# Optimization experiments

Hardware: AMD Instinct MI355X
Metric: run time of the kernel (lower is better)

Reference implementation:

```python
import jax, jax.numpy as jnp
import numpy as np

N_NODES = 98304
N_EDGES = 1572864
HIDDEN = 64
N_COMM = 128


def setup_inputs() -> dict:
    key = jax.random.key(0)
    ks = jax.random.split(key, 9)
    return {
        "x_real": jax.random.normal(ks[0], (N_NODES, 1), dtype=jnp.float32),
        "x_imag": jax.random.normal(ks[1], (N_NODES, 1), dtype=jnp.float32),
        "edge_index": jax.random.randint(ks[2], (2, N_EDGES), 0, N_NODES),
        "edge_weight": jax.random.normal(ks[3], (N_EDGES,), dtype=jnp.float32),
        "comm_id": jax.random.randint(ks[4], (N_NODES,), 0, N_COMM),
        "W_local_r": jax.random.normal(ks[5], (HIDDEN, 1), dtype=jnp.float32) * 0.5,
        "W_local_i": jax.random.normal(ks[6], (HIDDEN, 1), dtype=jnp.float32) * 0.5,
        "W_global_r": jax.random.normal(ks[7], (HIDDEN, 1), dtype=jnp.float32) * 0.5,
        "W_global_i": jax.random.normal(ks[8], (HIDDEN, 1), dtype=jnp.float32) * 0.5,
    }


def reference(x_real, x_imag, edge_index, edge_weight, comm_id,
              W_local_r, W_local_i, W_global_r, W_global_i):
    """IntraInterCommunityBlock forward (combine='sum'), complex math as (real, imag) pairs.

    CommunityGNN (1 layer, no bias): complex Linear -> weighted scatter-add
    message passing -> CSiLU (SiLU applied independently to real and imag parts).
    Residual skipped because in_channels=1 != hidden (shape mismatch in source).
    Edge split by community is implemented by zero-masking edge weights, which is
    exactly equivalent for sum aggregation (message = w * x_j).
    """
    n = x_real.shape[0]
    src, dst = edge_index[0], edge_index[1]
    same = comm_id[src] == comm_id[dst]
    ew_intra = jnp.where(same, edge_weight, 0.0)
    ew_inter = jnp.where(same, 0.0, edge_weight)

    def gnn(Wr, Wi, ew):
        # complex linear: (Wr + iWi)(xr + i xi)
        hr = x_real @ Wr.T - x_imag @ Wi.T  # [N, H]
        hi = x_real @ Wi.T + x_imag @ Wr.T  # [N, H]
        # gather -> weight -> scatter-add (aggr='add')
        mr = ew[:, None] * hr[src]  # [E, H]
        mi = ew[:, None] * hi[src]
        ar = jax.ops.segment_sum(mr, dst, num_segments=n)
        ai = jax.ops.segment_sum(mi, dst, num_segments=n)
        # CSiLU: SiLU on real and imag parts
        return jax.nn.silu(ar), jax.nn.silu(ai)

    lr, li = gnn(W_local_r, W_local_i, ew_intra)
    gr, gi = gnn(W_global_r, W_global_i, ew_inter)
    # combine='sum'; stack real/imag on last axis -> [N, H, 2]
    return jnp.stack([lr + gr, li + gi], axis=-1)
```

## Files before the change

### kernel.cpp

```cpp
#include <hip/hip_runtime.h>

#define N_NODES 98304
#define N_EDGES 1572864
#define HIDDEN  64

#define NB      1536
#define NBLK    1536
#define CHUNK   1024
#define TPB     256
#define EPT     4
#define NBXC    (NB / 8)

#define FP_SCALE 1048576.0f
#define FP_INV   (1.0f / 1048576.0f)

__device__ __forceinline__ float silu_f(float x) {
    return x / (1.0f + __expf(-x));
}

__global__ __launch_bounds__(TPB) void prep_kernel(const float* __restrict__ xr,
                                                   const float* __restrict__ xi,
                                                   const int* __restrict__ comm,
                                                   float4* __restrict__ node)
{
    const int n = blockIdx.x * TPB + threadIdx.x;
    if (n < N_NODES) {
        float4 v;
        v.x = xr[n];
        v.y = xi[n];
        v.z = __int_as_float(comm[n]);
        v.w = 0.0f;
        node[n] = v;
    }
}

__global__ __launch_bounds__(TPB) void k_scatter(const int* __restrict__ ei,
    const float* __restrict__ ew, const float4* __restrict__ node,
    const int* __restrict__ comm,
    unsigned short* __restrict__ lbT, unsigned long long* __restrict__ payload)
{
    __shared__ unsigned long long sorted[CHUNK];
    __shared__ unsigned hist[NB];
    __shared__ unsigned localbase[NB];

    const int tid = threadIdx.x, blk = blockIdx.x;
    for (int i = tid; i < NB; i += TPB) hist[i] = 0;
    __syncthreads();

    const int ebase = blk * CHUNK;
    unsigned long long pay[EPT];
    unsigned pb[EPT], pr[EPT];
#pragma unroll
    for (int k = 0; k < EPT; ++k) {
        const int e = ebase + k * TPB + tid;
        const int s = ei[e];
        const int d = ei[N_EDGES + e];
        const float w = ew[e];
        const float4 ns = node[s];
        const int cd = comm[d];
        const int dr = __float2int_rn(w * ns.x * FP_SCALE);
        const int di = __float2int_rn(w * ns.y * FP_SCALE);
        const unsigned flag = (__float_as_int(ns.z) == cd) ? 0u : 1u;
        const unsigned b = (unsigned)d >> 6;
        pb[k] = b;
        pr[k] = atomicAdd(&hist[b], 1u);
        pay[k] = ((unsigned long long)((unsigned)dr & 0x07FFFFFFu) << 37)
               | ((unsigned long long)((unsigned)di & 0x07FFFFFFu) << 10)
               | ((unsigned long long)((unsigned)(d & 63)) << 4)
               | ((unsigned long long)flag << 1);
    }
    __syncthreads();

    if (tid < 64) {
        unsigned v[24];
        unsigned s = 0;
#pragma unroll
        for (int m = 0; m < 24; ++m) { v[m] = hist[tid * 24 + m]; s += v[m]; }
        unsigned p = s;
#pragma unroll
        for (int off = 1; off < 64; off <<= 1) {
            unsigned t = __shfl_up(p, off);
            if (tid >= off) p += t;
        }
        unsigned excl = p - s;
#pragma unroll
        for (int m = 0; m < 24; ++m) { unsigned t = v[m]; localbase[tid * 24 + m] = excl; excl += t; }
    }
    __syncthreads();

#pragma unroll
    for (int k = 0; k < EPT; ++k)
        sorted[localbase[pb[k]] + pr[k]] = pay[k];
    for (int i = tid; i < NB; i += TPB)
        lbT[(size_t)blk * NB + i] = (unsigned short)localbase[i];
    __syncthreads();

    const ulonglong2* src2 = (const ulonglong2*)sorted;
    ulonglong2* dst2 = (ulonglong2*)(payload + (size_t)blk * CHUNK);
#pragma unroll
    for (int i = tid; i < CHUNK / 2; i += TPB)
        dst2[i] = src2[i];
}

__global__ __launch_bounds__(TPB) void k_accum_final(
    const unsigned long long* __restrict__ payload,
    const unsigned short* __restrict__ lbT,
    const float* __restrict__ Wlr, const float* __restrict__ Wli,
    const float* __restrict__ Wgr, const float* __restrict__ Wgi,
    float4* __restrict__ out)
{
    __shared__ int accR[128];
    __shared__ int accI[128];
    __shared__ float2 w_s[4][32];
    const int tid = threadIdx.x, blk = blockIdx.x;
    const int bucket = (blk & 7) * NBXC + (blk >> 3);

    if (tid < 128) { accR[tid] = 0; accI[tid] = 0; }
    else {
        const int t = tid - 128;
        const int which = t >> 5, h2 = t & 31;
        const float* W = (which == 0) ? Wlr : (which == 1) ? Wli
                       : (which == 2) ? Wgr : Wgi;
        w_s[which][h2] = ((const float2*)W)[h2];
    }
    __syncthreads();

    for (int c = tid; c < NBLK; c += TPB) {
        const unsigned start = lbT[(size_t)c * NB + bucket];
        const unsigned end   = (bucket < NB - 1)
                             ? (unsigned)lbT[(size_t)c * NB + bucket + 1]
                             : (unsigned)CHUNK;
        const unsigned long long* chunkp = payload + (size_t)c * CHUNK;
        for (unsigned i = start; i < end; ++i) {
            const unsigned long long p = chunkp[i];
            const int dr = (int)((long long)p >> 37);
            const int di = (int)(((long long)(p << 27)) >> 37);
            const unsigned idx = (((unsigned)(p >> 4) & 63u) << 1) | ((unsigned)(p >> 1) & 1u);
            atomicAdd(&accR[idx], dr);
            atomicAdd(&accI[idx], di);
        }
    }
    __syncthreads();

    const size_t obase = (size_t)bucket * 2048;
#pragma unroll
    for (int jj = 0; jj < 8; ++jj) {
        const int idx = jj * 256 + tid;
        const int ln  = idx >> 5;
        const int h2  = idx & 31;
        const float sr_l = (float)accR[ln * 2 + 0] * FP_INV;
        const float si_l = (float)accI[ln * 2 + 0] * FP_INV;
        const float sr_g = (float)accR[ln * 2 + 1] * FP_INV;
        const float si_g = (float)accI[ln * 2 + 1] * FP_INV;
        const float2 a = w_s[0][h2], c = w_s[1][h2];
        const float2 g = w_s[2][h2], f = w_s[3][h2];
        float4 o;
        {
            const float arl = a.x * sr_l - c.x * si_l;
            const float ail = c.x * sr_l + a.x * si_l;
            const float arg = g.x * sr_g - f.x * si_g;
            const float aig = f.x * sr_g + g.x * si_g;
            o.x = silu_f(arl) + silu_f(arg);
            o.y = silu_f(ail) + silu_f(aig);
        }
        {
            const float arl = a.y * sr_l - c.y * si_l;
            const float ail = c.y * sr_l + a.y * si_l;
            const float arg = g.y * sr_g - f.y * si_g;
            const float aig = f.y * sr_g + g.y * si_g;
            o.z = silu_f(arl) + silu_f(arg);
            o.w = silu_f(ail) + silu_f(aig);
        }
        out[obase + idx] = o;
    }
}

__global__ void edge_scatter_fb(const int* __restrict__ ei,
                                const float* __restrict__ ew,
                                const int* __restrict__ comm,
                                const float* __restrict__ xr,
                                const float* __restrict__ xi,
                                unsigned long long* __restrict__ P)
{
    const int e = blockIdx.x * blockDim.x + threadIdx.x;
    if (e >= N_EDGES) return;
    const int s = ei[e];
    const int d = ei[N_EDGES + e];
    const float w = ew[e];
    const int dr = __float2int_rn(w * xr[s] * FP_SCALE);
    const int di = __float2int_rn(w * xi[s] * FP_SCALE);
    const unsigned long long delta =
        (unsigned long long)(((long long)dr << 32) + (long long)di);
    const int base = (comm[s] == comm[d]) ? 0 : N_NODES;
    atomicAdd(&P[base + d], delta);
}

__global__ void epilogue_fb(const unsigned long long* __restrict__ P,
                            const float* __restrict__ Wlr,
                            const float* __restrict__ Wli,
                            const float* __restrict__ Wgr,
                            const float* __restrict__ Wgi,
                            float4* __restrict__ out)
{
    const int total = N_NODES * (HIDDEN / 2);
    const int t = blockIdx.x * blockDim.x + threadIdx.x;
    if (t >= total) return;
    const int n = t >> 5, h2 = t & 31;
    float sr_l, si_l, sr_g, si_g;
    {
        const unsigned long long U = P[n];
        const int bi = (int)(unsigned)(U & 0xffffffffULL);
        const int ar = (int)(unsigned)(U >> 32) + (bi < 0 ? 1 : 0);
        sr_l = (float)ar * FP_INV; si_l = (float)bi * FP_INV;
    }
    {
        const unsigned long long U = P[N_NODES + n];
        const int bi = (int)(unsigned)(U & 0xffffffffULL);
        const int ar = (int)(unsigned)(U >> 32) + (bi < 0 ? 1 : 0);
        sr_g = (float)ar * FP_INV; si_g = (float)bi * FP_INV;
    }
    const float2 wlr = ((const float2*)Wlr)[h2];
    const float2 wli = ((const float2*)Wli)[h2];
    const float2 wgr = ((const float2*)Wgr)[h2];
    const float2 wgi = ((const float2*)Wgi)[h2];
    float4 o;
    {
        const float arl = wlr.x * sr_l - wli.x * si_l;
        const float ail = wli.x * sr_l + wlr.x * si_l;
        const float arg = wgr.x * sr_g - wgi.x * si_g;
        const float aig = wgi.x * sr_g + wgr.x * si_g;
        o.x = silu_f(arl) + silu_f(arg);
        o.y = silu_f(ail) + silu_f(aig);
    }
    {
        const float arl = wlr.y * sr_l - wli.y * si_l;
        const float ail = wli.y * sr_l + wlr.y * si_l;
        const float arg = wgr.y * sr_g - wgi.y * si_g;
        const float aig = wgi.y * sr_g + wgr.y * si_g;
        o.z = silu_f(arl) + silu_f(arg);
        o.w = silu_f(ail) + silu_f(aig);
    }
    out[t] = o;
}

extern "C" void kernel_launch(void* const* d_in, const int* in_sizes, int n_in,
                              void* d_out, int out_size, void* d_ws, size_t ws_size,
                              hipStream_t stream) {
    const float* xr   = (const float*)d_in[0];
    const float* xi   = (const float*)d_in[1];
    const int*   ei   = (const int*)d_in[2];
    const float* ew   = (const float*)d_in[3];
    const int*   comm = (const int*)d_in[4];
    const float* Wlr  = (const float*)d_in[5];
    const float* Wli  = (const float*)d_in[6];
    const float* Wgr  = (const float*)d_in[7];
    const float* Wgi  = (const float*)d_in[8];

    const size_t payload_bytes = (size_t)N_EDGES * sizeof(unsigned long long);
    const size_t lbT_bytes     = (size_t)NBLK * NB * sizeof(unsigned short);
    const size_t node_bytes    = (size_t)N_NODES * sizeof(float4);
    const size_t need = payload_bytes + lbT_bytes + node_bytes;

    if (ws_size >= need) {
        char* p = (char*)d_ws;
        unsigned long long* payload = (unsigned long long*)p;  p += payload_bytes;
        unsigned short* lbT         = (unsigned short*)p;      p += lbT_bytes;
        float4* node                = (float4*)p;

        hipLaunchKernelGGL(prep_kernel, dim3(N_NODES / TPB), dim3(TPB), 0, stream,
                           xr, xi, comm, node);
        hipLaunchKernelGGL(k_scatter, dim3(NBLK), dim3(TPB), 0, stream,
                           ei, ew, node, comm, lbT, payload);
        hipLaunchKernelGGL(k_accum_final, dim3(NB), dim3(TPB), 0, stream,
                           payload, lbT, Wlr, Wli, Wgr, Wgi, (float4*)d_out);
    } else {
        unsigned long long* P = (unsigned long long*)d_ws;
        hipMemsetAsync(P, 0, (size_t)2 * N_NODES * sizeof(unsigned long long), stream);
        hipLaunchKernelGGL(edge_scatter_fb, dim3((N_EDGES + 255) / 256), dim3(256), 0, stream,
                           ei, ew, comm, xr, xi, P);
        const int total = N_NODES * (HIDDEN / 2);
        hipLaunchKernelGGL(epilogue_fb, dim3((total + 255) / 256), dim3(256), 0, stream,
                           P, Wlr, Wli, Wgr, Wgi, (float4*)d_out);
    }
}
```

Before: 64.72 us.

## Transpose bucket offsets into packed rows and drop node-packing prep kernel

Adds a transpose kernel that turns the per-chunk bucket offset table into per-bucket rows, packing start and count into one 16-bit word. The accumulate kernel then reads its bucket's row contiguously instead of doing strided loads across chunks, and skips empty chunks early. It also removes the prep kernel that packed nodes into float4, gathering xr, xi and comm directly in the scatter kernel, and uses nontemporal loads for the edge streams. In exchange there is an extra kernel launch, more uncoalesced gathers in the scatter kernel, and a fallback read of the original table when a count saturates.

```diff
diff --git a/kernel.cpp b/kernel.cpp
--- a/kernel.cpp
+++ b/kernel.cpp
@@ -18,25 +18,9 @@
     return x / (1.0f + __expf(-x));
 }
 
-__global__ __launch_bounds__(TPB) void prep_kernel(const float* __restrict__ xr,
-                                                   const float* __restrict__ xi,
-                                                   const int* __restrict__ comm,
-                                                   float4* __restrict__ node)
-{
-    const int n = blockIdx.x * TPB + threadIdx.x;
-    if (n < N_NODES) {
-        float4 v;
-        v.x = xr[n];
-        v.y = xi[n];
-        v.z = __int_as_float(comm[n]);
-        v.w = 0.0f;
-        node[n] = v;
-    }
-}
-
 __global__ __launch_bounds__(TPB) void k_scatter(const int* __restrict__ ei,
-    const float* __restrict__ ew, const float4* __restrict__ node,
-    const int* __restrict__ comm,
+    const float* __restrict__ ew, const float* __restrict__ xr,
+    const float* __restrict__ xi, const int* __restrict__ comm,
     unsigned short* __restrict__ lbT, unsigned long long* __restrict__ payload)
 {
     __shared__ unsigned long long sorted[CHUNK];
@@ -53,14 +37,12 @@
 #pragma unroll
     for (int k = 0; k < EPT; ++k) {
         const int e = ebase + k * TPB + tid;
-        const int s = ei[e];
-        const int d = ei[N_EDGES + e];
-        const float w = ew[e];
-        const float4 ns = node[s];
-        const int cd = comm[d];
-        const int dr = __float2int_rn(w * ns.x * FP_SCALE);
-        const int di = __float2int_rn(w * ns.y * FP_SCALE);
-        const unsigned flag = (__float_as_int(ns.z) == cd) ? 0u : 1u;
+        const int s = __builtin_nontemporal_load(&ei[e]);
+        const int d = __builtin_nontemporal_load(&ei[N_EDGES + e]);
+        const float w = __builtin_nontemporal_load(&ew[e]);
+        const int dr = __float2int_rn(w * xr[s] * FP_SCALE);
+        const int di = __float2int_rn(w * xi[s] * FP_SCALE);
+        const unsigned flag = (comm[s] == comm[d]) ? 0u : 1u;
         const unsigned b = (unsigned)d >> 6;
         pb[k] = b;
         pr[k] = atomicAdd(&hist[b], 1u);
@@ -102,8 +84,38 @@
         dst2[i] = src2[i];
 }
 
+__global__ __launch_bounds__(TPB) void k_transpose(
+    const unsigned short* __restrict__ lbT,
+    unsigned short* __restrict__ lbTT)
+{
+    __shared__ unsigned short t[64][66];
+    const int b0 = blockIdx.x * 64;
+    const int c0 = blockIdx.y * 64;
+    const int tid = threadIdx.x;
+
+    for (int idx = tid; idx < 64 * 65; idx += TPB) {
+        const int r  = idx / 65;
+        const int cb = idx % 65;
+        const int gb = b0 + cb;
+        t[r][cb] = (gb < NB) ? lbT[(size_t)(c0 + r) * NB + gb]
+                             : (unsigned short)CHUNK;
+    }
+    __syncthreads();
+
+    for (int idx = tid; idx < 64 * 64; idx += TPB) {
+        const int col = idx >> 6;
+        const int r   = idx & 63;
+        const unsigned start = t[r][col];
+        unsigned cnt = (unsigned)t[r][col + 1] - start;
+        if (cnt > 63u) cnt = 63u;
+        const unsigned pk = cnt ? ((start << 6) | cnt) : 0u;
+        lbTT[(size_t)(b0 + col) * NBLK + (c0 + r)] = (unsigned short)pk;
+    }
+}
+
 __global__ __launch_bounds__(TPB) void k_accum_final(
     const unsigned long long* __restrict__ payload,
+    const unsigned short* __restrict__ lbTT,
     const unsigned short* __restrict__ lbT,
     const float* __restrict__ Wlr, const float* __restrict__ Wli,
     const float* __restrict__ Wgr, const float* __restrict__ Wgi,
@@ -125,11 +137,17 @@
     }
     __syncthreads();
 
+    const unsigned short* row = lbTT + (size_t)bucket * NBLK;
     for (int c = tid; c < NBLK; c += TPB) {
-        const unsigned start = lbT[(size_t)c * NB + bucket];
-        const unsigned end   = (bucket < NB - 1)
-                             ? (unsigned)lbT[(size_t)c * NB + bucket + 1]
-                             : (unsigned)CHUNK;
+        const unsigned pk = row[c];
+        if (pk == 0u) continue;
+        const unsigned start = pk >> 6;
+        unsigned end = start + (pk & 63u);
+        if ((pk & 63u) == 63u) {
+            end = (bucket < NB - 1)
+                ? (unsigned)lbT[(size_t)c * NB + bucket + 1]
+                : (unsigned)CHUNK;
+        }
         const unsigned long long* chunkp = payload + (size_t)c * CHUNK;
         for (unsigned i = start; i < end; ++i) {
             const unsigned long long p = chunkp[i];
@@ -258,21 +276,21 @@
 
     const size_t payload_bytes = (size_t)N_EDGES * sizeof(unsigned long long);
     const size_t lbT_bytes     = (size_t)NBLK * NB * sizeof(unsigned short);
-    const size_t node_bytes    = (size_t)N_NODES * sizeof(float4);
-    const size_t need = payload_bytes + lbT_bytes + node_bytes;
+    const size_t lbTT_bytes    = (size_t)NB * NBLK * sizeof(unsigned short);
+    const size_t need = payload_bytes + lbT_bytes + lbTT_bytes;
 
     if (ws_size >= need) {
         char* p = (char*)d_ws;
         unsigned long long* payload = (unsigned long long*)p;  p += payload_bytes;
         unsigned short* lbT         = (unsigned short*)p;      p += lbT_bytes;
-        float4* node                = (float4*)p;
-
-        hipLaunchKernelGGL(prep_kernel, dim3(N_NODES / TPB), dim3(TPB), 0, stream,
-                           xr, xi, comm, node);
+        unsigned short* lbTT        = (unsigned short*)p;
+
         hipLaunchKernelGGL(k_scatter, dim3(NBLK), dim3(TPB), 0, stream,
-                           ei, ew, node, comm, lbT, payload);
+                           ei, ew, xr, xi, comm, lbT, payload);
+        hipLaunchKernelGGL(k_transpose, dim3(NB / 64, NBLK / 64), dim3(TPB), 0, stream,
+                           lbT, lbTT);
         hipLaunchKernelGGL(k_accum_final, dim3(NB), dim3(TPB), 0, stream,
-                           payload, lbT, Wlr, Wli, Wgr, Wgi, (float4*)d_out);
+                           payload, lbTT, lbT, Wlr, Wli, Wgr, Wgi, (float4*)d_out);
     } else {
         unsigned long long* P = (unsigned long long*)d_ws;
         hipMemsetAsync(P, 0, (size_t)2 * N_NODES * sizeof(unsigned long long), stream);
```

New measurement: 74.26 us. 1.15x slower.

## Transpose bucket offsets and build shared worklist for balanced accumulation

Applied to the files above, without the earlier changes.

Adds a transpose kernel that converts the per-chunk bucket offset table into a per-bucket row, packing start and count into one 16-bit value. The accumulate kernel can then read that row contiguously. It compacts all edge indices for its bucket into a shared-memory worklist and spreads them evenly across threads, replacing per-thread serial loops over uneven ranges. The cost is an extra kernel launch and extra traffic for the transposed table. The worklist is capped at a fixed capacity, so entries past the cap would be silently dropped if a bucket is oversized. The transposed table also reuses the workspace region previously used for node data, which is safe only because the scatter kernel has already finished with it.

```diff
diff --git a/kernel.cpp b/kernel.cpp
--- a/kernel.cpp
+++ b/kernel.cpp
@@ -10,6 +10,7 @@
 #define TPB     256
 #define EPT     4
 #define NBXC    (NB / 8)
+#define WLCAP   1600
 
 #define FP_SCALE 1048576.0f
 #define FP_INV   (1.0f / 1048576.0f)
@@ -102,8 +103,38 @@
         dst2[i] = src2[i];
 }
 
+__global__ __launch_bounds__(TPB) void k_transpose(
+    const unsigned short* __restrict__ lbT,
+    unsigned short* __restrict__ lbTT)
+{
+    __shared__ unsigned short t[64][66];
+    const int b0 = blockIdx.x * 64;
+    const int c0 = blockIdx.y * 64;
+    const int tid = threadIdx.x;
+
+    for (int idx = tid; idx < 64 * 65; idx += TPB) {
+        const int r  = idx / 65;
+        const int cb = idx % 65;
+        const int gb = b0 + cb;
+        t[r][cb] = (gb < NB) ? lbT[(size_t)(c0 + r) * NB + gb]
+                             : (unsigned short)CHUNK;
+    }
+    __syncthreads();
+
+    for (int idx = tid; idx < 64 * 64; idx += TPB) {
+        const int col = idx >> 6;
+        const int r   = idx & 63;
+        const unsigned start = t[r][col];
+        unsigned cnt = (unsigned)t[r][col + 1] - start;
+        if (cnt > 63u) cnt = 63u;
+        const unsigned pk = cnt ? ((start << 6) | cnt) : 0u;
+        lbTT[(size_t)(b0 + col) * NBLK + (c0 + r)] = (unsigned short)pk;
+    }
+}
+
 __global__ __launch_bounds__(TPB) void k_accum_final(
     const unsigned long long* __restrict__ payload,
+    const unsigned short* __restrict__ lbTT,
     const unsigned short* __restrict__ lbT,
     const float* __restrict__ Wlr, const float* __restrict__ Wli,
     const float* __restrict__ Wgr, const float* __restrict__ Wgi,
@@ -112,33 +143,50 @@
     __shared__ int accR[128];
     __shared__ int accI[128];
     __shared__ float2 w_s[4][32];
+    __shared__ unsigned wl[WLCAP];
+    __shared__ unsigned wcnt;
     const int tid = threadIdx.x, blk = blockIdx.x;
     const int bucket = (blk & 7) * NBXC + (blk >> 3);
 
     if (tid < 128) { accR[tid] = 0; accI[tid] = 0; }
-    else {
+    else if (tid < 256) {
         const int t = tid - 128;
         const int which = t >> 5, h2 = t & 31;
         const float* W = (which == 0) ? Wlr : (which == 1) ? Wli
                        : (which == 2) ? Wgr : Wgi;
         w_s[which][h2] = ((const float2*)W)[h2];
     }
-    __syncthreads();
-
+    if (tid == 0) wcnt = 0;
+    __syncthreads();
+
+    const unsigned short* row = lbTT + (size_t)bucket * NBLK;
     for (int c = tid; c < NBLK; c += TPB) {
-        const unsigned start = lbT[(size_t)c * NB + bucket];
-        const unsigned end   = (bucket < NB - 1)
-                             ? (unsigned)lbT[(size_t)c * NB + bucket + 1]
-                             : (unsigned)CHUNK;
-        const unsigned long long* chunkp = payload + (size_t)c * CHUNK;
-        for (unsigned i = start; i < end; ++i) {
-            const unsigned long long p = chunkp[i];
-            const int dr = (int)((long long)p >> 37);
-            const int di = (int)(((long long)(p << 27)) >> 37);
-            const unsigned idx = (((unsigned)(p >> 4) & 63u) << 1) | ((unsigned)(p >> 1) & 1u);
-            atomicAdd(&accR[idx], dr);
-            atomicAdd(&accI[idx], di);
+        const unsigned pk = row[c];
+        if (pk == 0u) continue;
+        const unsigned start = pk >> 6;
+        unsigned cnt = pk & 63u;
+        if (cnt == 63u) {
+            const unsigned end = (bucket < NB - 1)
+                ? (unsigned)lbT[(size_t)c * NB + bucket + 1]
+                : (unsigned)CHUNK;
+            cnt = end - start;
         }
+        const unsigned base = atomicAdd(&wcnt, cnt);
+        const unsigned gidx = (unsigned)c * CHUNK + start;
+        for (unsigned j = 0; j < cnt; ++j)
+            if (base + j < WLCAP) wl[base + j] = gidx + j;
+    }
+    __syncthreads();
+
+    unsigned n = wcnt;
+    if (n > WLCAP) n = WLCAP;
+    for (unsigned i = tid; i < n; i += TPB) {
+        const unsigned long long p = payload[wl[i]];
+        const int dr = (int)((long long)p >> 37);
+        const int di = (int)(((long long)(p << 27)) >> 37);
+        const unsigned idx = (((unsigned)(p >> 4) & 63u) << 1) | ((unsigned)(p >> 1) & 1u);
+        atomicAdd(&accR[idx], dr);
+        atomicAdd(&accI[idx], di);
     }
     __syncthreads();
 
@@ -258,21 +306,24 @@
 
     const size_t payload_bytes = (size_t)N_EDGES * sizeof(unsigned long long);
     const size_t lbT_bytes     = (size_t)NBLK * NB * sizeof(unsigned short);
-    const size_t node_bytes    = (size_t)N_NODES * sizeof(float4);
-    const size_t need = payload_bytes + lbT_bytes + node_bytes;
+    const size_t shared_bytes  = (size_t)NB * NBLK * sizeof(unsigned short);
+    const size_t need = payload_bytes + lbT_bytes + shared_bytes;
 
     if (ws_size >= need) {
         char* p = (char*)d_ws;
         unsigned long long* payload = (unsigned long long*)p;  p += payload_bytes;
         unsigned short* lbT         = (unsigned short*)p;      p += lbT_bytes;
         float4* node                = (float4*)p;
+        unsigned short* lbTT        = (unsigned short*)p;
 
         hipLaunchKernelGGL(prep_kernel, dim3(N_NODES / TPB), dim3(TPB), 0, stream,
                            xr, xi, comm, node);
         hipLaunchKernelGGL(k_scatter, dim3(NBLK), dim3(TPB), 0, stream,
                            ei, ew, node, comm, lbT, payload);
+        hipLaunchKernelGGL(k_transpose, dim3(NB / 64, NBLK / 64), dim3(TPB), 0, stream,
+                           lbT, lbTT);
         hipLaunchKernelGGL(k_accum_final, dim3(NB), dim3(TPB), 0, stream,
-                           payload, lbT, Wlr, Wli, Wgr, Wgi, (float4*)d_out);
+                           payload, lbTT, lbT, Wlr, Wli, Wgr, Wgi, (float4*)d_out);
     } else {
         unsigned long long* P = (unsigned long long*)d_ws;
         hipMemsetAsync(P, 0, (size_t)2 * N_NODES * sizeof(unsigned long long), stream);
```

After: 74.77 us. +15.5%, slower.
